# Optimization experiments

Measured on AMD Instinct MI355X. Metric: run time of the kernel, lower is better.

The kernel has to match this reference:

```python
import jax, jax.numpy as jnp
import numpy as np

B, D, C = 4096, 2048, 64
L_HP, D_HP, OMEGA, EPSILON = 0.5, 1.0, 100.0, 0.1
LN_EPS = 1e-5
CLASS_COUNTS = [5000,4500,4050,3645,3280,2952,2657,2391,2152,1937,1743,1569,1412,1271,1144,1029,926,834,750,675,608,547,492,443,399,359,323,291,262,236,212,191,172,155,139,125,113,101,91,82,74,66,60,54,48,43,39,35,32,28,26,23,21,19,17,15,14,12,11,10,9,8,7,7]


def setup_inputs() -> dict:
    key = jax.random.key(0)
    k_x, k_y, k_b, k_u1, k_u2 = jax.random.split(key, 5)
    counts = jnp.asarray(CLASS_COUNTS, dtype=jnp.float32)
    # set_class_weights: tilde_C = 1/log(counts*d + eps), min-max normalized, scaled by l
    tilde = 1.0 / jnp.log(counts * D_HP + EPSILON)
    c = (tilde - jnp.min(tilde)) / (jnp.max(tilde) - jnp.min(tilde)) * L_HP
    # set_fs_classes: 1 where count <= omega
    fs_classes = jnp.where(counts <= OMEGA, 1, 0).astype(jnp.int32)
    x = jax.random.normal(k_x, (B, D), dtype=jnp.float32)
    y = jax.random.randint(k_y, (B,), 0, C)
    beta_idx = jax.random.randint(k_b, (B,), 0, B)
    u1 = jax.random.uniform(k_u1, (B,))
    u2 = jax.random.uniform(k_u2, (B,))
    alpha = jnp.where(u1 > 0.5, u2, jnp.ones((B,), jnp.float32))
    return {"x": x, "y": y, "alpha": alpha, "beta_idx": beta_idx, "c": c, "fs_classes": fs_classes}


def reference(x, y, alpha, beta_idx, c, fs_classes):
    n_batch, dim = x.shape
    num_classes = c.shape[0]
    # --- reconstruct ---
    mu = jnp.mean(x, axis=-1, keepdims=True)
    var = jnp.mean((x - mu) ** 2, axis=-1, keepdims=True)
    x_norm = (x - mu) / jnp.sqrt(var + LN_EPS) / jnp.sqrt(jnp.asarray(dim, x.dtype))
    sim = jnp.matmul(x_norm, x_norm.T)  # [B, B]
    # E[i, j] = eye[i, j] + fs_mask[j]  (broadcast over rows), thresholded to {0, 1}
    fs_mask = fs_classes[y].astype(x.dtype)  # [B]
    E = jnp.eye(n_batch, dtype=x.dtype) + fs_mask[None, :]
    E = jnp.where(E >= 1.0, 1.0, 0.0)
    sim = jax.nn.softmax(sim - 100000.0 * E, axis=-1)
    contrib = c[y]  # [B]
    reconstructions = jnp.matmul(sim, x)  # [B, D]
    R = reconstructions * contrib[:, None] + x * (1.0 - contrib)[:, None]
    # --- pairwise_mix: M @ R with M[i,:] = alpha[i]*e_i + (1-alpha[i])*e_{beta_idx[i]} ---
    y_oh = jax.nn.one_hot(y, num_classes, dtype=x.dtype)
    a = alpha[:, None]
    x_mix = a * R + (1.0 - a) * R[beta_idx]
    y_mix = a * y_oh + (1.0 - a) * y_oh[beta_idx]
    return (x_mix, y_mix)
```

## Files before the change

### kernel.cpp

```cpp
#include <hip/hip_runtime.h>
#include <cstdint>
#include <cstddef>

typedef __bf16 bf16;
typedef __bf16 bf16x8 __attribute__((ext_vector_type(8)));
typedef float floatx4 __attribute__((ext_vector_type(4)));
typedef int intx8 __attribute__((ext_vector_type(8)));

#define NB 4096
#define ND 2048
#define NCLS 64
#define TSTRIDE 144
#define OS 136

__device__ __forceinline__ void stage16(const void* g, void* l) {
  __builtin_amdgcn_global_load_lds(
      (__attribute__((address_space(1))) unsigned int*)g,
      (__attribute__((address_space(3))) unsigned int*)l, 16, 0, 0);
}

__device__ __forceinline__ unsigned char fp8x1(float f) {
  return (unsigned char)(__builtin_amdgcn_cvt_pk_fp8_f32(f, f, 0, false) & 0xFF);
}
__device__ __forceinline__ int fp8x4(float f0, float f1, float f2, float f3) {
  int d = __builtin_amdgcn_cvt_pk_fp8_f32(f0, f1, 0, false);
  return __builtin_amdgcn_cvt_pk_fp8_f32(f2, f3, d, true);
}

__device__ __forceinline__ void stage_step(const unsigned char* __restrict__ A,
                                           const unsigned char* __restrict__ B,
                                           int K, int m0, int n0, int k0,
                                           unsigned char* As,
                                           unsigned char* Bs) {
  const int t = threadIdx.x;
  const int w = t >> 6, lane = t & 63;
#pragma unroll
  for (int q = 0; q < 4; ++q) {
    const int slot = w * 256 + q * 64 + lane;
    const int row = slot >> 3;
    const int cc = (slot & 7) ^ (row & 7);
    stage16(A + (size_t)(m0 + row) * K + (k0 + cc * 16),
            As + (w * 256 + q * 64) * 16);
  }
#pragma unroll
  for (int q = 0; q < 4; ++q) {
    const int slot = w * 256 + q * 64 + lane;
    const int row = slot >> 3;
    const int cc = (slot & 7) ^ (row & 7);
    stage16(B + (size_t)(n0 + row) * K + (k0 + cc * 16),
            Bs + (w * 256 + q * 64) * 16);
  }
}

__device__ __forceinline__ void gemm_core8(const unsigned char* __restrict__ A,
                                           const unsigned char* __restrict__ B,
                                           int K, int m0, int n0,
                                           unsigned char* As0, unsigned char* Bs0,
                                           unsigned char* As1, unsigned char* Bs1,
                                           floatx4 acc[4][4]) {
  const int t = threadIdx.x;
  const int w = t >> 6;
  const int lane = t & 63;
  const int wm = w >> 1, wn = w & 1;
  const int lm = lane & 15, quad = lane >> 4;
  const int nk = K >> 7;

  stage_step(A, B, K, m0, n0, 0, As0, Bs0);

  for (int k = 0; k < nk; ++k) {
    __syncthreads();
    if (k + 1 < nk)
      stage_step(A, B, K, m0, n0, (k + 1) << 7, (k & 1) ? As0 : As1,
                 (k & 1) ? Bs0 : Bs1);
    unsigned char* Ac = (k & 1) ? As1 : As0;
    unsigned char* Bc = (k & 1) ? Bs1 : Bs0;

    intx8 af[4], bfr[4];
#pragma unroll
    for (int i = 0; i < 4; ++i) {
      const int row = wm * 64 + i * 16 + lm;
      const int c0 = (quad * 2) ^ (row & 7);
      const int4 lo = *(const int4*)(Ac + row * 128 + c0 * 16);
      const int4 hi = *(const int4*)(Ac + row * 128 + (c0 ^ 1) * 16);
      af[i][0] = lo.x; af[i][1] = lo.y; af[i][2] = lo.z; af[i][3] = lo.w;
      af[i][4] = hi.x; af[i][5] = hi.y; af[i][6] = hi.z; af[i][7] = hi.w;
    }
#pragma unroll
    for (int i = 0; i < 4; ++i) {
      const int row = wn * 64 + i * 16 + lm;
      const int c0 = (quad * 2) ^ (row & 7);
      const int4 lo = *(const int4*)(Bc + row * 128 + c0 * 16);
      const int4 hi = *(const int4*)(Bc + row * 128 + (c0 ^ 1) * 16);
      bfr[i][0] = lo.x; bfr[i][1] = lo.y; bfr[i][2] = lo.z; bfr[i][3] = lo.w;
      bfr[i][4] = hi.x; bfr[i][5] = hi.y; bfr[i][6] = hi.z; bfr[i][7] = hi.w;
    }
#pragma unroll
    for (int mi = 0; mi < 4; ++mi)
#pragma unroll
      for (int ni = 0; ni < 4; ++ni)
        acc[mi][ni] = __builtin_amdgcn_mfma_scale_f32_16x16x128_f8f6f4(
            af[mi], bfr[ni], acc[mi][ni], 0, 0, 0, 127, 0, 127);
  }
}


__global__ __launch_bounds__(256) void prep_kernel(
    const float* __restrict__ x, const int* __restrict__ y,
    const float* __restrict__ c, const int* __restrict__ fs,
    unsigned char* __restrict__ XN8, unsigned char* __restrict__ XBT8,
    float* __restrict__ lrow, float* __restrict__ contrib,
    int* __restrict__ maskcol) {
  __shared__ float tile[64][65];
  const int t = threadIdx.x;

  if (blockIdx.x < NB) {
    const int row = blockIdx.x;
    const float4* xr = (const float4*)(x + (size_t)row * ND);
    float4 v0 = xr[t], v1 = xr[t + 256];
    float s = v0.x + v0.y + v0.z + v0.w + v1.x + v1.y + v1.z + v1.w;
    float q = v0.x * v0.x + v0.y * v0.y + v0.z * v0.z + v0.w * v0.w +
              v1.x * v1.x + v1.y * v1.y + v1.z * v1.z + v1.w * v1.w;
#pragma unroll
    for (int o = 32; o > 0; o >>= 1) {
      s += __shfl_down(s, o);
      q += __shfl_down(q, o);
    }
    const int w = t >> 6;
    if ((t & 63) == 0) { tile[0][w] = s; tile[1][w] = q; }
    __syncthreads();
    s = tile[0][0] + tile[0][1] + tile[0][2] + tile[0][3];
    q = tile[1][0] + tile[1][1] + tile[1][2] + tile[1][3];
    const float mu = s * (1.0f / ND);
    const float var = q * (1.0f / ND) - mu * mu;
    const float sc =
        rsqrtf(var + 1e-5f) * 0.02209708691207961f * 32.0f;

    int* orow = (int*)(XN8 + (size_t)row * ND);
    orow[t] = fp8x4((v0.x - mu) * sc, (v0.y - mu) * sc, (v0.z - mu) * sc,
                    (v0.w - mu) * sc);
    orow[256 + t] = fp8x4((v1.x - mu) * sc, (v1.y - mu) * sc, (v1.z - mu) * sc,
                          (v1.w - mu) * sc);

    if (t == 0) {
      lrow[row] = 0.0f;
      const int yi = y[row];
      contrib[row] = c[yi];
      maskcol[row] = fs[yi];
    }
  } else {
    const int b2 = blockIdx.x - NB;
    const int rb = b2 & 63;
    const int cb = b2 >> 6;
    const int tx = t & 63, ty = t >> 6;
#pragma unroll
    for (int rr = ty; rr < 64; rr += 4)
      tile[rr][tx] = x[(size_t)(rb * 64 + rr) * ND + cb * 64 + tx];
    __syncthreads();
    const int ro = t >> 2;
    const int co = t & 3;
    int4 v;
    {
      const int j = co * 16;
      v.x = fp8x4(tile[j + 0][ro], tile[j + 1][ro], tile[j + 2][ro], tile[j + 3][ro]);
      v.y = fp8x4(tile[j + 4][ro], tile[j + 5][ro], tile[j + 6][ro], tile[j + 7][ro]);
      v.z = fp8x4(tile[j + 8][ro], tile[j + 9][ro], tile[j + 10][ro], tile[j + 11][ro]);
      v.w = fp8x4(tile[j + 12][ro], tile[j + 13][ro], tile[j + 14][ro], tile[j + 15][ro]);
    }
    *(int4*)(XBT8 + (size_t)(cb * 64 + ro) * NB + rb * 64 + co * 16) = v;
  }
}

__global__ __launch_bounds__(256) void gemm_sim_kernel(
    const unsigned char* __restrict__ XN8, unsigned char* __restrict__ P8,
    float* __restrict__ lrow, const int* __restrict__ maskcol) {
  __shared__ unsigned char smem[65536];
  unsigned char* As0 = smem;
  unsigned char* Bs0 = smem + 16384;
  unsigned char* As1 = smem + 32768;
  unsigned char* Bs1 = smem + 49152;

  const int b = blockIdx.x;
  int bj = (int)((sqrtf(8.0f * (float)b + 1.0f) - 1.0f) * 0.5f);
  while ((bj + 1) * (bj + 2) / 2 <= b) ++bj;
  while (bj * (bj + 1) / 2 > b) --bj;
  const int bi = b - bj * (bj + 1) / 2;
  const int m0 = bi * 128, n0 = bj * 128;

  floatx4 acc[4][4];
#pragma unroll
  for (int i = 0; i < 4; ++i)
#pragma unroll
    for (int j = 0; j < 4; ++j) acc[i][j] = 0.0f;

  gemm_core8(XN8, XN8, ND, m0, n0, As0, Bs0, As1, Bs1, acc);

  const int t = threadIdx.x, w = t >> 6, lane = t & 63;
  const int wm = w >> 1, wn = w & 1, lm = lane & 15, quad = lane >> 4;

  int cmj[4];
#pragma unroll
  for (int ni = 0; ni < 4; ++ni) cmj[ni] = maskcol[n0 + wn * 64 + ni * 16 + lm];
  int rmk[4][4];
#pragma unroll
  for (int mi = 0; mi < 4; ++mi)
#pragma unroll
    for (int r = 0; r < 4; ++r)
      rmk[mi][r] = maskcol[m0 + wm * 64 + mi * 16 + quad * 4 + r];

  float rs[4][4];
#pragma unroll
  for (int mi = 0; mi < 4; ++mi)
#pragma unroll
    for (int r = 0; r < 4; ++r) rs[mi][r] = 0.0f;

#pragma unroll
  for (int ni = 0; ni < 4; ++ni) {
    const int gcol = n0 + wn * 64 + ni * 16 + lm;
#pragma unroll
    for (int mi = 0; mi < 4; ++mi) {
#pragma unroll
      for (int r = 0; r < 4; ++r) {
        const int grow = m0 + wm * 64 + mi * 16 + quad * 4 + r;
        float e = (grow == gcol) ? 0.0f
                                 : __expf(acc[mi][ni][r] * 0.0009765625f);
        acc[mi][ni][r] = e;
        rs[mi][r] += cmj[ni] ? 0.0f : e;
      }
    }
  }
#pragma unroll
  for (int mi = 0; mi < 4; ++mi)
#pragma unroll
    for (int r = 0; r < 4; ++r) {
      float vsum = rs[mi][r];
      vsum += __shfl_xor(vsum, 1);
      vsum += __shfl_xor(vsum, 2);
      vsum += __shfl_xor(vsum, 4);
      vsum += __shfl_xor(vsum, 8);
      if (lm == 0)
        atomicAdd(&lrow[m0 + wm * 64 + mi * 16 + quad * 4 + r], vsum);
    }

  __syncthreads();
#pragma unroll
  for (int ni = 0; ni < 4; ++ni) {
    const int col = wn * 64 + ni * 16 + lm;
#pragma unroll
    for (int mi = 0; mi < 4; ++mi)
#pragma unroll
      for (int r = 0; r < 4; ++r) {
        const int row = wm * 64 + mi * 16 + quad * 4 + r;
        smem[row * TSTRIDE + col] = fp8x1(cmj[ni] ? 0.0f : acc[mi][ni][r]);
      }
  }
  __syncthreads();
#pragma unroll
  for (int it = 0; it < 4; ++it) {
    const int row = it * 32 + (t >> 3), ch = t & 7;
    int4 v = *(const int4*)(smem + row * TSTRIDE + ch * 16);
    *(int4*)(P8 + (size_t)(m0 + row) * NB + n0 + ch * 16) = v;
  }

  if (bi != bj) {
    __syncthreads();
#pragma unroll
    for (int ni = 0; ni < 4; ++ni) {
      const int tc = wn * 64 + ni * 16 + lm;
      float cs = 0.0f;
#pragma unroll
      for (int mi = 0; mi < 4; ++mi) {
        float g0 = rmk[mi][0] ? 0.0f : acc[mi][ni][0];
        float g1 = rmk[mi][1] ? 0.0f : acc[mi][ni][1];
        float g2 = rmk[mi][2] ? 0.0f : acc[mi][ni][2];
        float g3 = rmk[mi][3] ? 0.0f : acc[mi][ni][3];
        cs += g0 + g1 + g2 + g3;
        *(int*)(smem + tc * TSTRIDE + wm * 64 + mi * 16 + quad * 4) =
            fp8x4(g0, g1, g2, g3);
      }
      cs += __shfl_xor(cs, 16);
      cs += __shfl_xor(cs, 32);
      if (quad == 0) atomicAdd(&lrow[n0 + tc], cs);
    }
    __syncthreads();
#pragma unroll
    for (int it = 0; it < 4; ++it) {
      const int row = it * 32 + (t >> 3), ch = t & 7;
      int4 v = *(const int4*)(smem + row * TSTRIDE + ch * 16);
      *(int4*)(P8 + (size_t)(n0 + row) * NB + m0 + ch * 16) = v;
    }
  }
}

__global__ __launch_bounds__(256) void gemm_recon_kernel(
    const unsigned char* __restrict__ P8, const unsigned char* __restrict__ XBT8,
    const float* __restrict__ x, const float* __restrict__ lrow,
    const float* __restrict__ contrib, bf16* __restrict__ R) {
  __shared__ unsigned char smem[65536];
  unsigned char* As0 = smem;
  unsigned char* Bs0 = smem + 16384;
  unsigned char* As1 = smem + 32768;
  unsigned char* Bs1 = smem + 49152;

  const int id = blockIdx.x;
  const int xcd = id & 7;
  const int s = id >> 3;
  const int bx = xcd * 2 + (s & 1);
  const int by = s >> 1;
  const int m0 = by * 128, n0 = bx * 128;

  floatx4 acc[4][4];
#pragma unroll
  for (int i = 0; i < 4; ++i)
#pragma unroll
    for (int j = 0; j < 4; ++j) acc[i][j] = 0.0f;

  gemm_core8(P8, XBT8, NB, m0, n0, As0, Bs0, As1, Bs1, acc);

  const int t = threadIdx.x, w = t >> 6, lane = t & 63;
  const int wm = w >> 1, wn = w & 1, lm = lane & 15, quad = lane >> 4;

  __syncthreads();
  bf16* osm = (bf16*)smem;
#pragma unroll
  for (int mi = 0; mi < 4; ++mi) {
#pragma unroll
    for (int r = 0; r < 4; ++r) {
      const int lrow_i = wm * 64 + mi * 16 + quad * 4 + r;
      const int grow = m0 + lrow_i;
      const float inv = 1.0f / lrow[grow];
      const float ci = contrib[grow];
#pragma unroll
      for (int ni = 0; ni < 4; ++ni) {
        const int lcol = wn * 64 + ni * 16 + lm;
        const float rec = acc[mi][ni][r] * inv;
        const float xv = x[(size_t)grow * ND + n0 + lcol];
        osm[lrow_i * OS + lcol] = (bf16)(rec * ci + xv * (1.0f - ci));
      }
    }
  }
  __syncthreads();
#pragma unroll
  for (int it = 0; it < 8; ++it) {
    const int row = it * 16 + (t >> 4), ch = t & 15;
    int4 v = *(const int4*)(osm + row * OS + ch * 8);
    *(int4*)(R + (size_t)(m0 + row) * ND + n0 + ch * 8) = v;
  }
}

__global__ __launch_bounds__(256) void mix_kernel(
    const bf16* __restrict__ R, const float* __restrict__ alpha,
    const int* __restrict__ beta_idx, const int* __restrict__ y,
    float* __restrict__ out) {
  const int i = blockIdx.x, t = threadIdx.x;
  const float a = alpha[i];
  const int bi = beta_idx[i];
  const bf16x8* Ri = (const bf16x8*)(R + (size_t)i * ND);
  const bf16x8* Rb = (const bf16x8*)(R + (size_t)bi * ND);
  const float b = 1.0f - a;
  bf16x8 r = Ri[t], g = Rb[t];
  float4 o0, o1;
  o0.x = a * (float)r[0] + b * (float)g[0];
  o0.y = a * (float)r[1] + b * (float)g[1];
  o0.z = a * (float)r[2] + b * (float)g[2];
  o0.w = a * (float)r[3] + b * (float)g[3];
  o1.x = a * (float)r[4] + b * (float)g[4];
  o1.y = a * (float)r[5] + b * (float)g[5];
  o1.z = a * (float)r[6] + b * (float)g[6];
  o1.w = a * (float)r[7] + b * (float)g[7];
  float4* o = (float4*)(out + (size_t)i * ND + t * 8);
  o[0] = o0;
  o[1] = o1;
  if (t < NCLS) {
    const int yi = y[i], yb = y[bi];
    const float v = a * (t == yi ? 1.0f : 0.0f) + b * (t == yb ? 1.0f : 0.0f);
    out[(size_t)NB * ND + (size_t)i * NCLS + t] = v;
  }
}

extern "C" void kernel_launch(void* const* d_in, const int* in_sizes, int n_in,
                              void* d_out, int out_size, void* d_ws,
                              size_t ws_size, hipStream_t stream) {
  const float* x = (const float*)d_in[0];
  const int* y = (const int*)d_in[1];
  const float* alpha = (const float*)d_in[2];
  const int* beta = (const int*)d_in[3];
  const float* c = (const float*)d_in[4];
  const int* fs = (const int*)d_in[5];
  float* out = (float*)d_out;
  char* ws = (char*)d_ws;

  unsigned char* XN8  = (unsigned char*)(ws + 0);
  unsigned char* XBT8 = (unsigned char*)(ws + 8388608);
  unsigned char* P8   = (unsigned char*)(ws + 16777216);
  bf16* R   = (bf16*)(ws + 33554432);
  float* LR = (float*)(ws + 50331648);
  float* CT = (float*)(ws + 50331648 + 16384);
  int* MC   = (int*)(ws + 50331648 + 32768);

  prep_kernel<<<NB + 2048, 256, 0, stream>>>(x, y, c, fs, XN8, XBT8, LR, CT, MC);
  gemm_sim_kernel<<<528, 256, 0, stream>>>(XN8, P8, LR, MC);
  gemm_recon_kernel<<<512, 256, 0, stream>>>(P8, XBT8, x, LR, CT, R);
  mix_kernel<<<NB, 256, 0, stream>>>(R, alpha, beta, y, out);
}
```

Measured before the change: 180.9 us.

## Compact unmasked columns via permutation to shrink sim and recon GEMM K dimension

Adds a single-block kernel that builds a permutation of the rows whose class is not few-shot, pads it to a multiple of 128, and records the count. The similarity GEMM now computes only rows × kept columns, dropping the symmetric triangular scheme and its transposed write-back. The recon GEMM's K loop now runs only over the compacted columns, and the transposed X is gathered through the permutation. This skips the work on masked columns, which contribute zero after softmax. In exchange it gives up the symmetry reuse, computes the full rectangle instead, and adds an extra serial launch.

```diff
diff --git a/kernel.cpp b/kernel.cpp
--- a/kernel.cpp
+++ b/kernel.cpp
@@ -27,51 +27,51 @@
   return __builtin_amdgcn_cvt_pk_fp8_f32(f2, f3, d, true);
 }
 
-__device__ __forceinline__ void stage_step(const unsigned char* __restrict__ A,
-                                           const unsigned char* __restrict__ B,
-                                           int K, int m0, int n0, int k0,
-                                           unsigned char* As,
-                                           unsigned char* Bs) {
+__device__ __forceinline__ void stage_step2(const unsigned char* const* ap,
+                                            const unsigned char* const* bp,
+                                            int k0, unsigned char* As,
+                                            unsigned char* Bs) {
+  const int w = threadIdx.x >> 6;
+#pragma unroll
+  for (int q = 0; q < 4; ++q)
+    stage16(ap[q] + k0, As + (w * 256 + q * 64) * 16);
+#pragma unroll
+  for (int q = 0; q < 4; ++q)
+    stage16(bp[q] + k0, Bs + (w * 256 + q * 64) * 16);
+}
+
+__device__ __forceinline__ void make_ptrs(const unsigned char* base,
+                                          size_t stride, int r0,
+                                          const unsigned char** p) {
   const int t = threadIdx.x;
   const int w = t >> 6, lane = t & 63;
-#pragma unroll
-  for (int q = 0; q < 4; ++q) {
-    const int slot = w * 256 + q * 64 + lane;
-    const int row = slot >> 3;
-    const int cc = (slot & 7) ^ (row & 7);
-    stage16(A + (size_t)(m0 + row) * K + (k0 + cc * 16),
-            As + (w * 256 + q * 64) * 16);
-  }
-#pragma unroll
-  for (int q = 0; q < 4; ++q) {
-    const int slot = w * 256 + q * 64 + lane;
-    const int row = slot >> 3;
-    const int cc = (slot & 7) ^ (row & 7);
-    stage16(B + (size_t)(n0 + row) * K + (k0 + cc * 16),
-            Bs + (w * 256 + q * 64) * 16);
-  }
-}
-
-__device__ __forceinline__ void gemm_core8(const unsigned char* __restrict__ A,
-                                           const unsigned char* __restrict__ B,
-                                           int K, int m0, int n0,
-                                           unsigned char* As0, unsigned char* Bs0,
-                                           unsigned char* As1, unsigned char* Bs1,
+  const int rq = lane >> 3;
+  const int coff = ((lane & 7) ^ rq) * 16;
+#pragma unroll
+  for (int q = 0; q < 4; ++q)
+    p[q] = base + (size_t)(r0 + w * 32 + q * 8 + rq) * stride + coff;
+}
+
+__device__ __forceinline__ void gemm_core8(const unsigned char* const* ap,
+                                           const unsigned char* const* bp,
+                                           int nk, unsigned char* As0,
+                                           unsigned char* Bs0,
+                                           unsigned char* As1,
+                                           unsigned char* Bs1,
                                            floatx4 acc[4][4]) {
   const int t = threadIdx.x;
   const int w = t >> 6;
   const int lane = t & 63;
   const int wm = w >> 1, wn = w & 1;
   const int lm = lane & 15, quad = lane >> 4;
-  const int nk = K >> 7;
-
-  stage_step(A, B, K, m0, n0, 0, As0, Bs0);
+
+  stage_step2(ap, bp, 0, As0, Bs0);
 
   for (int k = 0; k < nk; ++k) {
     __syncthreads();
     if (k + 1 < nk)
-      stage_step(A, B, K, m0, n0, (k + 1) << 7, (k & 1) ? As0 : As1,
-                 (k & 1) ? Bs0 : Bs1);
+      stage_step2(ap, bp, (k + 1) << 7, (k & 1) ? As0 : As1,
+                  (k & 1) ? Bs0 : Bs1);
     unsigned char* Ac = (k & 1) ? As1 : As0;
     unsigned char* Bc = (k & 1) ? Bs1 : Bs0;
 
@@ -104,12 +104,56 @@
 }
 
 
+__global__ __launch_bounds__(1024) void perm_kernel(
+    const int* __restrict__ y, const int* __restrict__ fs,
+    const float* __restrict__ c, int* __restrict__ perm,
+    int* __restrict__ minfo, float* __restrict__ lrow,
+    float* __restrict__ contrib) {
+  const int t = threadIdx.x;
+  const int base = t * 4;
+  int fl[4];
+  int cnt = 0;
+#pragma unroll
+  for (int j = 0; j < 4; ++j) {
+    const int yi = y[base + j];
+    fl[j] = (fs[yi] == 0) ? 1 : 0;
+    cnt += fl[j];
+    contrib[base + j] = c[yi];
+    lrow[base + j] = 0.0f;
+  }
+  const int lane = t & 63, w = t >> 6;
+  int inc = cnt;
+#pragma unroll
+  for (int o = 1; o < 64; o <<= 1) {
+    int v = __shfl_up(inc, o);
+    if (lane >= o) inc += v;
+  }
+  __shared__ int wsum[16];
+  __shared__ int Msh;
+  if (lane == 63) wsum[w] = inc;
+  __syncthreads();
+  int wbase = 0;
+  for (int i = 0; i < w; ++i) wbase += wsum[i];
+  int pos = wbase + inc - cnt;
+#pragma unroll
+  for (int j = 0; j < 4; ++j)
+    if (fl[j]) perm[pos++] = base + j;
+  if (t == 1023) Msh = wbase + inc;
+  __syncthreads();
+  const int M = Msh;
+  const int Mp = (M + 127) & ~127;
+  if (t < Mp - M) perm[M + t] = 0;
+  if (t == 0) {
+    minfo[0] = M;
+    minfo[1] = Mp;
+    minfo[2] = Mp >> 7;
+  }
+}
+
 __global__ __launch_bounds__(256) void prep_kernel(
-    const float* __restrict__ x, const int* __restrict__ y,
-    const float* __restrict__ c, const int* __restrict__ fs,
-    unsigned char* __restrict__ XN8, unsigned char* __restrict__ XBT8,
-    float* __restrict__ lrow, float* __restrict__ contrib,
-    int* __restrict__ maskcol) {
+    const float* __restrict__ x, unsigned char* __restrict__ XN8,
+    unsigned char* __restrict__ XBT8, const int* __restrict__ perm,
+    const int* __restrict__ minfo) {
   __shared__ float tile[64][65];
   const int t = threadIdx.x;
 
@@ -140,21 +184,15 @@
                     (v0.w - mu) * sc);
     orow[256 + t] = fp8x4((v1.x - mu) * sc, (v1.y - mu) * sc, (v1.z - mu) * sc,
                           (v1.w - mu) * sc);
-
-    if (t == 0) {
-      lrow[row] = 0.0f;
-      const int yi = y[row];
-      contrib[row] = c[yi];
-      maskcol[row] = fs[yi];
-    }
   } else {
     const int b2 = blockIdx.x - NB;
     const int rb = b2 & 63;
     const int cb = b2 >> 6;
+    if (rb * 64 >= minfo[1]) return;
     const int tx = t & 63, ty = t >> 6;
 #pragma unroll
     for (int rr = ty; rr < 64; rr += 4)
-      tile[rr][tx] = x[(size_t)(rb * 64 + rr) * ND + cb * 64 + tx];
+      tile[rr][tx] = x[(size_t)perm[rb * 64 + rr] * ND + cb * 64 + tx];
     __syncthreads();
     const int ro = t >> 2;
     const int co = t & 3;
@@ -172,19 +210,34 @@
 
 __global__ __launch_bounds__(256) void gemm_sim_kernel(
     const unsigned char* __restrict__ XN8, unsigned char* __restrict__ P8,
-    float* __restrict__ lrow, const int* __restrict__ maskcol) {
+    float* __restrict__ lrow, const int* __restrict__ perm,
+    const int* __restrict__ minfo) {
   __shared__ unsigned char smem[65536];
   unsigned char* As0 = smem;
   unsigned char* Bs0 = smem + 16384;
   unsigned char* As1 = smem + 32768;
   unsigned char* Bs1 = smem + 49152;
 
-  const int b = blockIdx.x;
-  int bj = (int)((sqrtf(8.0f * (float)b + 1.0f) - 1.0f) * 0.5f);
-  while ((bj + 1) * (bj + 2) / 2 <= b) ++bj;
-  while (bj * (bj + 1) / 2 > b) --bj;
-  const int bi = b - bj * (bj + 1) / 2;
-  const int m0 = bi * 128, n0 = bj * 128;
+  const int Mp = minfo[1];
+  const int bi = blockIdx.x >> 5;
+  const int bjc = blockIdx.x & 31;
+  const int n0 = bjc * 128;
+  if (n0 >= Mp) return;
+  const int M = minfo[0];
+  const int m0 = bi * 128;
+
+  const int t = threadIdx.x, w = t >> 6, lane = t & 63;
+  const int rq = lane >> 3;
+  const int coff = ((lane & 7) ^ rq) * 16;
+
+  const unsigned char* ap[4];
+  const unsigned char* bp[4];
+#pragma unroll
+  for (int q = 0; q < 4; ++q) {
+    const int row = w * 32 + q * 8 + rq;
+    ap[q] = XN8 + (size_t)(m0 + row) * ND + coff;
+    bp[q] = XN8 + (size_t)perm[n0 + row] * ND + coff;
+  }
 
   floatx4 acc[4][4];
 #pragma unroll
@@ -192,39 +245,36 @@
 #pragma unroll
     for (int j = 0; j < 4; ++j) acc[i][j] = 0.0f;
 
-  gemm_core8(XN8, XN8, ND, m0, n0, As0, Bs0, As1, Bs1, acc);
-
-  const int t = threadIdx.x, w = t >> 6, lane = t & 63;
+  gemm_core8(ap, bp, ND >> 7, As0, Bs0, As1, Bs1, acc);
+
   const int wm = w >> 1, wn = w & 1, lm = lane & 15, quad = lane >> 4;
 
-  int cmj[4];
-#pragma unroll
-  for (int ni = 0; ni < 4; ++ni) cmj[ni] = maskcol[n0 + wn * 64 + ni * 16 + lm];
-  int rmk[4][4];
+  int pcol[4], valid[4];
+#pragma unroll
+  for (int ni = 0; ni < 4; ++ni) {
+    const int gc = n0 + wn * 64 + ni * 16 + lm;
+    valid[ni] = (gc < M) ? 1 : 0;
+    pcol[ni] = perm[gc];
+  }
+
+  float rs[4][4];
 #pragma unroll
   for (int mi = 0; mi < 4; ++mi)
 #pragma unroll
-    for (int r = 0; r < 4; ++r)
-      rmk[mi][r] = maskcol[m0 + wm * 64 + mi * 16 + quad * 4 + r];
-
-  float rs[4][4];
-#pragma unroll
-  for (int mi = 0; mi < 4; ++mi)
-#pragma unroll
     for (int r = 0; r < 4; ++r) rs[mi][r] = 0.0f;
 
 #pragma unroll
   for (int ni = 0; ni < 4; ++ni) {
-    const int gcol = n0 + wn * 64 + ni * 16 + lm;
 #pragma unroll
     for (int mi = 0; mi < 4; ++mi) {
 #pragma unroll
       for (int r = 0; r < 4; ++r) {
         const int grow = m0 + wm * 64 + mi * 16 + quad * 4 + r;
-        float e = (grow == gcol) ? 0.0f
-                                 : __expf(acc[mi][ni][r] * 0.0009765625f);
+        const float e = (valid[ni] && grow != pcol[ni])
+                            ? __expf(acc[mi][ni][r] * 0.0009765625f)
+                            : 0.0f;
         acc[mi][ni][r] = e;
-        rs[mi][r] += cmj[ni] ? 0.0f : e;
+        rs[mi][r] += e;
       }
     }
   }
@@ -250,7 +300,7 @@
 #pragma unroll
       for (int r = 0; r < 4; ++r) {
         const int row = wm * 64 + mi * 16 + quad * 4 + r;
-        smem[row * TSTRIDE + col] = fp8x1(cmj[ni] ? 0.0f : acc[mi][ni][r]);
+        smem[row * TSTRIDE + col] = fp8x1(acc[mi][ni][r]);
       }
   }
   __syncthreads();
@@ -260,41 +310,13 @@
     int4 v = *(const int4*)(smem + row * TSTRIDE + ch * 16);
     *(int4*)(P8 + (size_t)(m0 + row) * NB + n0 + ch * 16) = v;
   }
-
-  if (bi != bj) {
-    __syncthreads();
-#pragma unroll
-    for (int ni = 0; ni < 4; ++ni) {
-      const int tc = wn * 64 + ni * 16 + lm;
-      float cs = 0.0f;
-#pragma unroll
-      for (int mi = 0; mi < 4; ++mi) {
-        float g0 = rmk[mi][0] ? 0.0f : acc[mi][ni][0];
-        float g1 = rmk[mi][1] ? 0.0f : acc[mi][ni][1];
-        float g2 = rmk[mi][2] ? 0.0f : acc[mi][ni][2];
-        float g3 = rmk[mi][3] ? 0.0f : acc[mi][ni][3];
-        cs += g0 + g1 + g2 + g3;
-        *(int*)(smem + tc * TSTRIDE + wm * 64 + mi * 16 + quad * 4) =
-            fp8x4(g0, g1, g2, g3);
-      }
-      cs += __shfl_xor(cs, 16);
-      cs += __shfl_xor(cs, 32);
-      if (quad == 0) atomicAdd(&lrow[n0 + tc], cs);
-    }
-    __syncthreads();
-#pragma unroll
-    for (int it = 0; it < 4; ++it) {
-      const int row = it * 32 + (t >> 3), ch = t & 7;
-      int4 v = *(const int4*)(smem + row * TSTRIDE + ch * 16);
-      *(int4*)(P8 + (size_t)(n0 + row) * NB + m0 + ch * 16) = v;
-    }
-  }
 }
 
 __global__ __launch_bounds__(256) void gemm_recon_kernel(
     const unsigned char* __restrict__ P8, const unsigned char* __restrict__ XBT8,
     const float* __restrict__ x, const float* __restrict__ lrow,
-    const float* __restrict__ contrib, bf16* __restrict__ R) {
+    const float* __restrict__ contrib, const int* __restrict__ minfo,
+    bf16* __restrict__ R) {
   __shared__ unsigned char smem[65536];
   unsigned char* As0 = smem;
   unsigned char* Bs0 = smem + 16384;
@@ -308,15 +330,27 @@
   const int by = s >> 1;
   const int m0 = by * 128, n0 = bx * 128;
 
+  const int t = threadIdx.x, w = t >> 6, lane = t & 63;
+  const int rq = lane >> 3;
+  const int coff = ((lane & 7) ^ rq) * 16;
+
+  const unsigned char* ap[4];
+  const unsigned char* bp[4];
+#pragma unroll
+  for (int q = 0; q < 4; ++q) {
+    const int row = w * 32 + q * 8 + rq;
+    ap[q] = P8 + (size_t)(m0 + row) * NB + coff;
+    bp[q] = XBT8 + (size_t)(n0 + row) * NB + coff;
+  }
+
   floatx4 acc[4][4];
 #pragma unroll
   for (int i = 0; i < 4; ++i)
 #pragma unroll
     for (int j = 0; j < 4; ++j) acc[i][j] = 0.0f;
 
-  gemm_core8(P8, XBT8, NB, m0, n0, As0, Bs0, As1, Bs1, acc);
-
-  const int t = threadIdx.x, w = t >> 6, lane = t & 63;
+  gemm_core8(ap, bp, minfo[2], As0, Bs0, As1, Bs1, acc);
+
   const int wm = w >> 1, wn = w & 1, lm = lane & 15, quad = lane >> 4;
 
   __syncthreads();
@@ -395,10 +429,12 @@
   bf16* R   = (bf16*)(ws + 33554432);
   float* LR = (float*)(ws + 50331648);
   float* CT = (float*)(ws + 50331648 + 16384);
-  int* MC   = (int*)(ws + 50331648 + 32768);
-
-  prep_kernel<<<NB + 2048, 256, 0, stream>>>(x, y, c, fs, XN8, XBT8, LR, CT, MC);
-  gemm_sim_kernel<<<528, 256, 0, stream>>>(XN8, P8, LR, MC);
-  gemm_recon_kernel<<<512, 256, 0, stream>>>(P8, XBT8, x, LR, CT, R);
+  int* PERM = (int*)(ws + 50331648 + 32768);
+  int* MINFO = (int*)(ws + 50331648 + 49152);
+
+  perm_kernel<<<1, 1024, 0, stream>>>(y, fs, c, PERM, MINFO, LR, CT);
+  prep_kernel<<<NB + 2048, 256, 0, stream>>>(x, XN8, XBT8, PERM, MINFO);
+  gemm_sim_kernel<<<1024, 256, 0, stream>>>(XN8, P8, LR, PERM, MINFO);
+  gemm_recon_kernel<<<512, 256, 0, stream>>>(P8, XBT8, x, LR, CT, MINFO, R);
   mix_kernel<<<NB, 256, 0, stream>>>(R, alpha, beta, y, out);
 }
```

New measurement: 188.3 us. 4.1% more time.
